# Kernel optimization log

Measured on AMD Instinct MI355X. Metric: run time of the kernel, lower is better.

## Reference

```python
import jax, jax.numpy as jnp
import numpy as np

KH, KW = 7, 7            # extraction kernel
EH, EW = 5, 5            # effective (cropped) kernel
PAD = (KH - EH) // 2     # = 1
EPS = 1e-7


def _extract_patches(x):
    # x: [B,H,W,C] -> patches [B,Ho,Wo,KH,KW,C], stride 1, VALID padding
    B, H, Wd, C = x.shape
    Ho, Wo = H - KH + 1, Wd - KW + 1
    rows = []
    for i in range(KH):
        cols = [x[:, i:i + Ho, j:j + Wo, :] for j in range(KW)]
        rows.append(jnp.stack(cols, axis=3))          # [B,Ho,Wo,KW,C]
    return jnp.stack(rows, axis=3)                     # [B,Ho,Wo,KH,KW,C]


def _rotate_bilinear(patches, angles):
    # patches: [N,KH,KW,C]; angles: [N]. Mirrors tf.contrib.image
    # angles_to_projective_transforms + transform(BILINEAR, fill=0).
    # Note: the layer's det(matrix)==0 NEAREST fallback never fires (det==1).
    N = patches.shape[0]
    c, s = jnp.cos(angles), jnp.sin(angles)
    Wm1, Hm1 = jnp.float32(KW - 1), jnp.float32(KH - 1)
    xo = (Wm1 - (c * Wm1 - s * Hm1)) * 0.5
    yo = (Hm1 - (s * Wm1 + c * Hm1)) * 0.5
    scale = jnp.float32(1.0 + EPS)   # transforms /= transforms[:,8:9]+1e-7
    a0, a1, a2 = c / scale, -s / scale, xo / scale
    a3, a4, a5 = s / scale, c / scale, yo / scale
    yg, xg = jnp.meshgrid(jnp.arange(KH, dtype=jnp.float32),
                          jnp.arange(KW, dtype=jnp.float32), indexing='ij')
    x_in = a0[:, None, None] * xg + a1[:, None, None] * yg + a2[:, None, None]
    y_in = a3[:, None, None] * xg + a4[:, None, None] * yg + a5[:, None, None]
    x0f = jnp.floor(x_in); y0f = jnp.floor(y_in)
    wx1 = x_in - x0f; wx0 = 1.0 - wx1
    wy1 = y_in - y0f; wy0 = 1.0 - wy1
    x0 = x0f.astype(jnp.int32); x1 = x0 + 1
    y0 = y0f.astype(jnp.int32); y1 = y0 + 1
    nidx = jnp.arange(N)[:, None, None]

    def corner(yi, xi, w):
        valid = ((xi >= 0) & (xi < KW) & (yi >= 0) & (yi < KH)).astype(patches.dtype)
        v = patches[nidx, jnp.clip(yi, 0, KH - 1), jnp.clip(xi, 0, KW - 1)]
        return (w * valid)[..., None] * v

    return (corner(y0, x0, wy0 * wx0) + corner(y0, x1, wy0 * wx1) +
            corner(y1, x0, wy1 * wx0) + corner(y1, x1, wy1 * wx1))


def reference(x, W, b):
    B, H, Wd, C = x.shape
    patches = _extract_patches(x)                      # [B,Ho,Wo,KH,KW,C]
    _, Ho, Wo = patches.shape[:3]
    intensity = jnp.sum(patches, axis=-1)              # [B,Ho,Wo,KH,KW]
    row_idx = jnp.repeat(jnp.arange(KH, dtype=jnp.float32), KW)   # rowMulti
    col_idx = jnp.tile(jnp.arange(KW, dtype=jnp.float32), KH)     # colMulti
    flat = intensity.reshape(-1, KH * KW)              # [N, KH*KW]
    denom = jnp.sum(flat, -1) + EPS
    cr = jnp.sum(flat * row_idx, -1) / denom - (KH - 1) / 2.0
    cc = jnp.sum(flat * col_idx, -1) / denom - (KW - 1) / 2.0
    angle = jnp.arctan2(cr, cc + EPS)                  # [N]
    patches_n = patches.reshape(-1, KH, KW, C)         # [N,KH,KW,C]
    rot = _rotate_bilinear(patches_n, angle)
    rot = rot[:, PAD:PAD + EH, PAD:PAD + EW, :]        # crop to effective
    rot = rot.reshape(B, Ho, Wo, EH * EW * C)
    w_flat = W.reshape(W.shape[0], -1)                 # [F, EH*EW*C]
    out = jnp.einsum('bhwk,fk->bhwf', rot, w_flat) + b
    return out


def setup_inputs() -> dict:
    key = jax.random.key(0)
    kx, kw, _ = jax.random.split(key, 3)
    x = jax.random.normal(kx, (8, 64, 64, 32), dtype=jnp.float32)
    W = jax.random.normal(kw, (64, EH, EW, 32), dtype=jnp.float32) * 0.05
    b = jnp.zeros((64,), dtype=jnp.float32)
    return {"x": x, "W": W, "b": b}
```

## Files before the change

### kernel.cpp

```cpp
#include <hip/hip_runtime.h>
#include <hip/hip_bf16.h>

#define KHH 7
#define KWW 7
#define EHH 5
#define EWW 5
#define EPSF 1e-7f
#define B_ 8
#define H_ 64
#define W_ 64
#define C_ 32
#define HO 58
#define WO 58
#define NPIX (B_*HO*WO)
#define NF 64
#define KDIM 800

typedef __bf16 v8bf __attribute__((ext_vector_type(8)));
typedef __bf16 v4bf __attribute__((ext_vector_type(4)));
typedef float  v4f  __attribute__((ext_vector_type(4)));

__global__ void k_chansum(const float* __restrict__ x, float* __restrict__ S) {
    int p = blockIdx.x*256 + threadIdx.x;
    if (p >= B_*H_*W_) return;
    const float4* xp = (const float4*)(x + (size_t)p*C_);
    float s = 0.f;
#pragma unroll
    for (int q = 0; q < 8; q++) { float4 v = xp[q]; s += v.x+v.y+v.z+v.w; }
    S[p] = s;
}

__global__ void k_wpack(const float* __restrict__ W, __bf16* __restrict__ Wp) {
    int t = blockIdx.x*256 + threadIdx.x;
    int j = t & 7; int lane = (t >> 3) & 63; int rest = t >> 9;
    int kb = rest % 25; int nt = rest / 25;
    int f = nt*16 + (lane & 15);
    int k = kb*32 + (lane >> 4)*8 + j;
    Wp[t] = (__bf16)W[f*KDIM + k];
}

__global__ void k_params(const float* __restrict__ S, float4* __restrict__ prm) {
    int pix = blockIdx.x*256 + threadIdx.x;
    if (pix >= NPIX) return;
    int b  = pix / (HO*WO); int rem = pix % (HO*WO);
    int ho = rem / WO;      int wo  = rem % WO;
    const float* Sp = S + (b*H_ + ho)*W_ + wo;
    float den = 0.f, crn = 0.f, ccn = 0.f;
#pragma unroll
    for (int i = 0; i < 7; i++) {
#pragma unroll
        for (int j = 0; j < 7; j++) {
            float v = Sp[i*W_ + j];
            den += v; crn += v*(float)i; ccn += v*(float)j;
        }
    }
    float dt = den + EPSF;
    float cr = crn/dt - 3.0f;
    float cc = ccn/dt - 3.0f;
    float ang = atan2f(cr, cc + EPSF);
    float c = cosf(ang), s = sinf(ang);
    const float scale = 1.0f + EPSF;
    float xo = (6.0f - (c*6.0f - s*6.0f))*0.5f;
    float yo = (6.0f - (s*6.0f + c*6.0f))*0.5f;
    prm[pix] = make_float4(c/scale, s/scale, xo/scale, yo/scale);
}

__global__ __launch_bounds__(256)
void k_main(const float* __restrict__ x, const v8bf* __restrict__ Wp,
            const float* __restrict__ bias, const float4* __restrict__ prm,
            float* __restrict__ out) {
    __shared__ float xt[7][22][32];
    __shared__ __bf16 rot[16][KDIM];
    __shared__ float4 pp[16];

    int tid = threadIdx.x;
    int wt = blockIdx.x, ho = blockIdx.y, b = blockIdx.z;
    int wo0 = wt*16;
    int npx = WO - wo0; if (npx > 16) npx = 16;
    int ncols = npx + 6;

    const float* xb = x + (size_t)((b*H_ + ho)*W_ + wo0)*C_;
    int total4 = 7*ncols*8;
    for (int e = tid; e < total4; e += 256) {
        int r = e/(ncols*8); int rem = e - r*(ncols*8);
        int cc = rem >> 3;   int q = rem & 7;
        *(float4*)&xt[r][cc][q*4] = *(const float4*)&xb[(r*W_ + cc)*C_ + q*4];
    }
    int pixbase = (b*HO + ho)*WO + wo0;
    if (tid < npx) pp[tid] = prm[pixbase + tid];
    __syncthreads();

    int tot = npx*200;
    for (int e = tid; e < tot; e += 256) {
        int px = e/200; int r4 = e - px*200;
        int pos = r4 >> 3; int ch4 = (r4 & 7)*4;
        int py = pos/5; int yy = py + 1; int xx = (pos - py*5) + 1;
        float4 p = pp[px];
        float xin = p.x*(float)xx - p.y*(float)yy + p.z;
        float yin = p.y*(float)xx + p.x*(float)yy + p.w;
        float x0f = floorf(xin), y0f = floorf(yin);
        float wx1 = xin - x0f, wx0 = 1.0f - wx1;
        float wy1 = yin - y0f, wy0 = 1.0f - wy1;
        int ix0 = (int)x0f, iy0 = (int)y0f;
        int ix1 = ix0 + 1,  iy1 = iy0 + 1;
        float a0=0.f, a1=0.f, a2=0.f, a3=0.f;
        auto corner = [&](int yi, int xi, float wgt) {
            bool valid = (xi >= 0) & (xi < KWW) & (yi >= 0) & (yi < KHH);
            float wv = valid ? wgt : 0.0f;
            int cy = yi < 0 ? 0 : (yi > 6 ? 6 : yi);
            int cx = xi < 0 ? 0 : (xi > 6 ? 6 : xi);
            float4 v = *(const float4*)&xt[cy][px + cx][ch4];
            a0 += wv*v.x; a1 += wv*v.y; a2 += wv*v.z; a3 += wv*v.w;
        };
        corner(iy0, ix0, wy0*wx0);
        corner(iy0, ix1, wy0*wx1);
        corner(iy1, ix0, wy1*wx0);
        corner(iy1, ix1, wy1*wx1);
        v4bf o; o[0]=(__bf16)a0; o[1]=(__bf16)a1; o[2]=(__bf16)a2; o[3]=(__bf16)a3;
        *(v4bf*)&rot[px][pos*32 + ch4] = o;
    }
    __syncthreads();

    int wv = tid >> 6; int lane = tid & 63;
    int m = lane & 15; int q = lane >> 4;
    v4f acc = {0.f, 0.f, 0.f, 0.f};
    const v8bf* wp = Wp + (size_t)wv*25*64;
#pragma unroll
    for (int kb = 0; kb < 25; kb++) {
        v8bf a = *(const v8bf*)&rot[m][kb*32 + q*8];
        v8bf bf = wp[kb*64 + lane];
        acc = __builtin_amdgcn_mfma_f32_16x16x32_bf16(a, bf, acc, 0, 0, 0);
    }
    int n = lane & 15; int f = wv*16 + n;
    float bv = bias[f];
#pragma unroll
    for (int r = 0; r < 4; r++) {
        int px = q*4 + r;
        if (px < npx) out[(size_t)(pixbase + px)*NF + f] = acc[r] + bv;
    }
}

extern "C" void kernel_launch(void* const* d_in, const int* in_sizes, int n_in,
                              void* d_out, int out_size, void* d_ws, size_t ws_size,
                              hipStream_t stream) {
    const float* x    = (const float*)d_in[0];
    const float* W    = (const float*)d_in[1];
    const float* bias = (const float*)d_in[2];
    float* out = (float*)d_out;
    char* ws = (char*)d_ws;
    float*  S   = (float*)ws;
    float4* prm = (float4*)(ws + 131072);
    __bf16* Wp  = (__bf16*)(ws + 131072 + 430592);

    k_chansum<<<dim3((B_*H_*W_)/256), 256, 0, stream>>>(x, S);
    k_wpack<<<dim3(200), 256, 0, stream>>>(W, Wp);
    k_params<<<dim3((NPIX + 255)/256), 256, 0, stream>>>(S, prm);
    k_main<<<dim3(4, HO, B_), 256, 0, stream>>>(x, (const v8bf*)Wp, bias, prm, out);
}
```

Measured before the change: 90.12 us.

## Fuse channel-sum and angle computation into main kernel, restructure rotation layout

Drops the separate channel-sum and parameter kernels and computes the per-pixel intensity sums and rotation angles inside the main kernel from the shared-memory input tile, cutting two launches and their global round-trips. The rotation stage now has one thread per (pixel, position) doing all 32 channels with the corner addresses and weights computed once, instead of eight threads repeating them. Shared-memory rows are padded to reduce bank conflicts, and the rotated buffer is laid out position-major. B fragments are preloaded into registers before the tile load. The costs are redundant angle work across neighbouring tiles, higher register pressure from the 32-float accumulator and 25 preloaded fragments, and fewer active threads in the rotation loop (400 items over 256 threads).

```diff
diff --git a/kernel.cpp b/kernel.cpp
--- a/kernel.cpp
+++ b/kernel.cpp
@@ -1,10 +1,6 @@
 #include <hip/hip_runtime.h>
 #include <hip/hip_bf16.h>
 
-#define KHH 7
-#define KWW 7
-#define EHH 5
-#define EWW 5
 #define EPSF 1e-7f
 #define B_ 8
 #define H_ 64
@@ -12,23 +8,14 @@
 #define C_ 32
 #define HO 58
 #define WO 58
-#define NPIX (B_*HO*WO)
 #define NF 64
 #define KDIM 800
 
+#define XTS 36
+#define RPS 520
+
 typedef __bf16 v8bf __attribute__((ext_vector_type(8)));
-typedef __bf16 v4bf __attribute__((ext_vector_type(4)));
 typedef float  v4f  __attribute__((ext_vector_type(4)));
-
-__global__ void k_chansum(const float* __restrict__ x, float* __restrict__ S) {
-    int p = blockIdx.x*256 + threadIdx.x;
-    if (p >= B_*H_*W_) return;
-    const float4* xp = (const float4*)(x + (size_t)p*C_);
-    float s = 0.f;
-#pragma unroll
-    for (int q = 0; q < 8; q++) { float4 v = xp[q]; s += v.x+v.y+v.z+v.w; }
-    S[p] = s;
-}
 
 __global__ void k_wpack(const float* __restrict__ W, __bf16* __restrict__ Wp) {
     int t = blockIdx.x*256 + threadIdx.x;
@@ -39,62 +26,74 @@
     Wp[t] = (__bf16)W[f*KDIM + k];
 }
 
-__global__ void k_params(const float* __restrict__ S, float4* __restrict__ prm) {
-    int pix = blockIdx.x*256 + threadIdx.x;
-    if (pix >= NPIX) return;
-    int b  = pix / (HO*WO); int rem = pix % (HO*WO);
-    int ho = rem / WO;      int wo  = rem % WO;
-    const float* Sp = S + (b*H_ + ho)*W_ + wo;
-    float den = 0.f, crn = 0.f, ccn = 0.f;
-#pragma unroll
-    for (int i = 0; i < 7; i++) {
-#pragma unroll
-        for (int j = 0; j < 7; j++) {
-            float v = Sp[i*W_ + j];
-            den += v; crn += v*(float)i; ccn += v*(float)j;
-        }
-    }
-    float dt = den + EPSF;
-    float cr = crn/dt - 3.0f;
-    float cc = ccn/dt - 3.0f;
-    float ang = atan2f(cr, cc + EPSF);
-    float c = cosf(ang), s = sinf(ang);
-    const float scale = 1.0f + EPSF;
-    float xo = (6.0f - (c*6.0f - s*6.0f))*0.5f;
-    float yo = (6.0f - (s*6.0f + c*6.0f))*0.5f;
-    prm[pix] = make_float4(c/scale, s/scale, xo/scale, yo/scale);
-}
-
 __global__ __launch_bounds__(256)
 void k_main(const float* __restrict__ x, const v8bf* __restrict__ Wp,
-            const float* __restrict__ bias, const float4* __restrict__ prm,
-            float* __restrict__ out) {
-    __shared__ float xt[7][22][32];
-    __shared__ __bf16 rot[16][KDIM];
+            const float* __restrict__ bias, float* __restrict__ out) {
+    __shared__ float  xt[7][22][XTS];
+    __shared__ __bf16 rot[25*RPS];
+    __shared__ float  Srow[7][22];
     __shared__ float4 pp[16];
 
     int tid = threadIdx.x;
+    int wv = tid >> 6, lane = tid & 63;
     int wt = blockIdx.x, ho = blockIdx.y, b = blockIdx.z;
     int wo0 = wt*16;
     int npx = WO - wo0; if (npx > 16) npx = 16;
     int ncols = npx + 6;
 
+    v8bf bfrag[25];
+    {
+        const v8bf* wp = Wp + (size_t)wv*25*64 + lane;
+#pragma unroll
+        for (int kb = 0; kb < 25; kb++) bfrag[kb] = wp[kb*64];
+    }
+
     const float* xb = x + (size_t)((b*H_ + ho)*W_ + wo0)*C_;
     int total4 = 7*ncols*8;
     for (int e = tid; e < total4; e += 256) {
         int r = e/(ncols*8); int rem = e - r*(ncols*8);
-        int cc = rem >> 3;   int q = rem & 7;
-        *(float4*)&xt[r][cc][q*4] = *(const float4*)&xb[(r*W_ + cc)*C_ + q*4];
+        int c = rem >> 3;    int q = rem & 7;
+        *(float4*)&xt[r][c][q*4] = *(const float4*)&xb[(r*W_ + c)*C_ + q*4];
     }
-    int pixbase = (b*HO + ho)*WO + wo0;
-    if (tid < npx) pp[tid] = prm[pixbase + tid];
     __syncthreads();
 
-    int tot = npx*200;
+    if (tid < 7*ncols) {
+        int r = tid / ncols, c = tid - r*ncols;
+        float s = 0.f;
+#pragma unroll
+        for (int q = 0; q < 8; q++) {
+            float4 v = *(const float4*)&xt[r][c][q*4];
+            s += v.x + v.y + v.z + v.w;
+        }
+        Srow[r][c] = s;
+    }
+    __syncthreads();
+
+    if (tid < npx) {
+        float den = 0.f, crn = 0.f, ccn = 0.f;
+#pragma unroll
+        for (int i = 0; i < 7; i++)
+#pragma unroll
+            for (int j = 0; j < 7; j++) {
+                float v = Srow[i][tid + j];
+                den += v; crn += v*(float)i; ccn += v*(float)j;
+            }
+        float dt = den + EPSF;
+        float cr = crn/dt - 3.0f;
+        float cc = ccn/dt - 3.0f;
+        float ang = atan2f(cr, cc + EPSF);
+        float c = cosf(ang), s = sinf(ang);
+        const float scale = 1.0f + EPSF;
+        float xo = (6.0f - (c*6.0f - s*6.0f))*0.5f;
+        float yo = (6.0f - (s*6.0f + c*6.0f))*0.5f;
+        pp[tid] = make_float4(c/scale, s/scale, xo/scale, yo/scale);
+    }
+    __syncthreads();
+
+    int tot = npx*25;
     for (int e = tid; e < tot; e += 256) {
-        int px = e/200; int r4 = e - px*200;
-        int pos = r4 >> 3; int ch4 = (r4 & 7)*4;
-        int py = pos/5; int yy = py + 1; int xx = (pos - py*5) + 1;
+        int px = e/25; int pos = e - px*25;
+        int py = pos/5; int yy = py + 1; int xx = pos - py*5 + 1;
         float4 p = pp[px];
         float xin = p.x*(float)xx - p.y*(float)yy + p.z;
         float yin = p.y*(float)xx + p.x*(float)yy + p.w;
@@ -103,40 +102,58 @@
         float wy1 = yin - y0f, wy0 = 1.0f - wy1;
         int ix0 = (int)x0f, iy0 = (int)y0f;
         int ix1 = ix0 + 1,  iy1 = iy0 + 1;
-        float a0=0.f, a1=0.f, a2=0.f, a3=0.f;
-        auto corner = [&](int yi, int xi, float wgt) {
-            bool valid = (xi >= 0) & (xi < KWW) & (yi >= 0) & (yi < KHH);
-            float wv = valid ? wgt : 0.0f;
+
+        const float* bp[4]; float wgt[4];
+        auto mkcorner = [&](int yi, int xi, float w, int idx) {
+            bool valid = (xi >= 0) & (xi < 7) & (yi >= 0) & (yi < 7);
             int cy = yi < 0 ? 0 : (yi > 6 ? 6 : yi);
             int cx = xi < 0 ? 0 : (xi > 6 ? 6 : xi);
-            float4 v = *(const float4*)&xt[cy][px + cx][ch4];
-            a0 += wv*v.x; a1 += wv*v.y; a2 += wv*v.z; a3 += wv*v.w;
+            bp[idx]  = &xt[cy][px + cx][0];
+            wgt[idx] = valid ? w : 0.0f;
         };
-        corner(iy0, ix0, wy0*wx0);
-        corner(iy0, ix1, wy0*wx1);
-        corner(iy1, ix0, wy1*wx0);
-        corner(iy1, ix1, wy1*wx1);
-        v4bf o; o[0]=(__bf16)a0; o[1]=(__bf16)a1; o[2]=(__bf16)a2; o[3]=(__bf16)a3;
-        *(v4bf*)&rot[px][pos*32 + ch4] = o;
+        mkcorner(iy0, ix0, wy0*wx0, 0);
+        mkcorner(iy0, ix1, wy0*wx1, 1);
+        mkcorner(iy1, ix0, wy1*wx0, 2);
+        mkcorner(iy1, ix1, wy1*wx1, 3);
+
+        float acc[32];
+#pragma unroll
+        for (int ch = 0; ch < 32; ch++) acc[ch] = 0.f;
+#pragma unroll
+        for (int cn = 0; cn < 4; cn++) {
+            const float* src = bp[cn]; float wq = wgt[cn];
+#pragma unroll
+            for (int q = 0; q < 8; q++) {
+                float4 v = *(const float4*)(src + q*4);
+                acc[q*4+0] += wq*v.x; acc[q*4+1] += wq*v.y;
+                acc[q*4+2] += wq*v.z; acc[q*4+3] += wq*v.w;
+            }
+        }
+        __bf16* dst = &rot[pos*RPS + px*32];
+#pragma unroll
+        for (int q8 = 0; q8 < 4; q8++) {
+            v8bf o;
+#pragma unroll
+            for (int j = 0; j < 8; j++) o[j] = (__bf16)acc[q8*8 + j];
+            *(v8bf*)&dst[q8*8] = o;
+        }
     }
     __syncthreads();
 
-    int wv = tid >> 6; int lane = tid & 63;
-    int m = lane & 15; int q = lane >> 4;
-    v4f acc = {0.f, 0.f, 0.f, 0.f};
-    const v8bf* wp = Wp + (size_t)wv*25*64;
+    int m = lane & 15, q = lane >> 4;
+    v4f acc4 = {0.f, 0.f, 0.f, 0.f};
 #pragma unroll
     for (int kb = 0; kb < 25; kb++) {
-        v8bf a = *(const v8bf*)&rot[m][kb*32 + q*8];
-        v8bf bf = wp[kb*64 + lane];
-        acc = __builtin_amdgcn_mfma_f32_16x16x32_bf16(a, bf, acc, 0, 0, 0);
+        v8bf a = *(const v8bf*)&rot[kb*RPS + m*32 + q*8];
+        acc4 = __builtin_amdgcn_mfma_f32_16x16x32_bf16(a, bfrag[kb], acc4, 0, 0, 0);
     }
-    int n = lane & 15; int f = wv*16 + n;
+    int f = wv*16 + m;
     float bv = bias[f];
+    int pixbase = (b*HO + ho)*WO + wo0;
 #pragma unroll
     for (int r = 0; r < 4; r++) {
         int px = q*4 + r;
-        if (px < npx) out[(size_t)(pixbase + px)*NF + f] = acc[r] + bv;
+        if (px < npx) out[(size_t)(pixbase + px)*NF + f] = acc4[r] + bv;
     }
 }
 
@@ -147,13 +164,8 @@
     const float* W    = (const float*)d_in[1];
     const float* bias = (const float*)d_in[2];
     float* out = (float*)d_out;
-    char* ws = (char*)d_ws;
-    float*  S   = (float*)ws;
-    float4* prm = (float4*)(ws + 131072);
-    __bf16* Wp  = (__bf16*)(ws + 131072 + 430592);
+    __bf16* Wp = (__bf16*)d_ws;
 
-    k_chansum<<<dim3((B_*H_*W_)/256), 256, 0, stream>>>(x, S);
     k_wpack<<<dim3(200), 256, 0, stream>>>(W, Wp);
-    k_params<<<dim3((NPIX + 255)/256), 256, 0, stream>>>(S, prm);
-    k_main<<<dim3(4, HO, B_), 256, 0, stream>>>(x, (const v8bf*)Wp, bias, prm, out);
+    k_main<<<dim3(4, HO, B_), 256, 0, stream>>>(x, (const v8bf*)Wp, bias, out);
 }
```

Measured after the change: 90.94 us. Within noise of the previous version (+0.9%).
